# Performance work log

Measured on AMD Instinct MI355X. Metric: run time of the kernel, lower is better.

The kernel has to match this reference:

```python
import jax, jax.numpy as jnp
import numpy as np


def setup_inputs() -> dict:
    key = jax.random.key(0)
    x = jax.random.normal(key, (16, 2048, 512), dtype=jnp.float32)
    return {"x": x}


def reference(x):
    # Cosine (L2-normalized) self-attention.
    # norm: [B, N, 1] L2 norm over feature dim
    norm = jnp.sqrt(jnp.sum(x * x, axis=2, keepdims=True))
    # scores[b, i, j] = <x_i, x_j> / (|x_i| |x_j|)  -> [B, N, N]
    scores = jnp.einsum('bnd,bmd->bnm', x, x) / (norm * jnp.swapaxes(norm, -2, -1))
    p_attn = jax.nn.softmax(scores, axis=-1)
    # output: [B, N, D]
    return jnp.einsum('bnm,bmd->bnd', p_attn, x)
```

## Files before the change

kernel.cpp:

```cpp
#include <hip/hip_runtime.h>
#include <hip/hip_bf16.h>
#include <cstdint>
#include <cstddef>

#define BB 16
#define NN 2048
#define DD 512

typedef _Float16 f16x8 __attribute__((ext_vector_type(8)));
typedef _Float16 f16x4 __attribute__((ext_vector_type(4)));
typedef float f32x4 __attribute__((ext_vector_type(4)));

__device__ __forceinline__ void async_ld16(void* lds, const void* g) {
    __builtin_amdgcn_global_load_lds(
        (const __attribute__((address_space(1))) unsigned int*)(uintptr_t)g,
        (__attribute__((address_space(3))) unsigned int*)(uint32_t)(uintptr_t)lds,
        16, 0, 0);
}

#define VM_WAIT(n) asm volatile("s_waitcnt vmcnt(" #n ")" ::: "memory")
#define RAW_BAR()  do { asm volatile("" ::: "memory"); __builtin_amdgcn_s_barrier(); asm volatile("" ::: "memory"); } while (0)
#define LGKM_BAR() do { asm volatile("s_waitcnt lgkmcnt(0)" ::: "memory"); \
                        __builtin_amdgcn_s_barrier();                      \
                        __builtin_amdgcn_sched_barrier(0); } while (0)
#define LGKM0_FENCE() do { asm volatile("s_waitcnt lgkmcnt(0)" ::: "memory"); \
                           __builtin_amdgcn_sched_barrier(0); } while (0)

__global__ __launch_bounds__(256) void k_prep(const float* __restrict__ x,
                                              _Float16* __restrict__ xhn,
                                              _Float16* __restrict__ vT,
                                              float* __restrict__ denom) {
    __shared__ _Float16 t[512 * 66];
    const int tid = threadIdx.x, lane = tid & 63, w = tid >> 6;
    const int b = blockIdx.y, j0 = blockIdx.x * 64;
    if (tid < 64) denom[b * NN + j0 + tid] = 0.f;
    const float* xb = x + ((size_t)b * NN + j0) * DD;

    for (int rr = 0; rr < 16; ++rr) {
        const int jj = w * 16 + rr;
        const float* xr = xb + (size_t)jj * DD;
        float4 a = ((const float4*)xr)[lane];
        float4 c = ((const float4*)xr)[lane + 64];
        float ss = a.x*a.x + a.y*a.y + a.z*a.z + a.w*a.w
                 + c.x*c.x + c.y*c.y + c.z*c.z + c.w*c.w;
        #pragma unroll
        for (int o = 1; o < 64; o <<= 1) ss += __shfl_xor(ss, o);
        const float rn = 1.0f / sqrtf(ss);
        _Float16* dst = xhn + ((size_t)b * NN + j0 + jj) * DD;
        f16x4 v0 = {(_Float16)(a.x*rn), (_Float16)(a.y*rn), (_Float16)(a.z*rn), (_Float16)(a.w*rn)};
        f16x4 v1 = {(_Float16)(c.x*rn), (_Float16)(c.y*rn), (_Float16)(c.z*rn), (_Float16)(c.w*rn)};
        *(f16x4*)(dst + 4 * lane) = v0;
        *(f16x4*)(dst + 256 + 4 * lane) = v1;
        const int d0 = 4 * lane, d1 = 256 + 4 * lane;
        t[(d0 + 0) * 66 + jj] = (_Float16)a.x;
        t[(d0 + 1) * 66 + jj] = (_Float16)a.y;
        t[(d0 + 2) * 66 + jj] = (_Float16)a.z;
        t[(d0 + 3) * 66 + jj] = (_Float16)a.w;
        t[(d1 + 0) * 66 + jj] = (_Float16)c.x;
        t[(d1 + 1) * 66 + jj] = (_Float16)c.y;
        t[(d1 + 2) * 66 + jj] = (_Float16)c.z;
        t[(d1 + 3) * 66 + jj] = (_Float16)c.w;
    }
    LGKM_BAR();
    #pragma unroll
    for (int it = 0; it < 16; ++it) {
        const int id = it * 256 + tid;
        const int d = id >> 3, ch = (id & 7) * 8;
        const uint32_t* tp = (const uint32_t*)&t[d * 66 + ch];
        uint4 v = {tp[0], tp[1], tp[2], tp[3]};
        *(uint4*)(vT + ((size_t)b * DD + d) * NN + j0 + ch) = v;
    }
}

__global__ __launch_bounds__(256) void k_scores(const _Float16* __restrict__ xhn,
                                                _Float16* __restrict__ W,
                                                float* __restrict__ denom) {
    __shared__ _Float16 smem[32768];
    const int tid = threadIdx.x;
    const int lane = tid & 63, wv = tid >> 6;
    const int wr = wv >> 1, wc = wv & 1;
    const int m_ = lane & 15, quad = lane >> 4;
    const int b = blockIdx.z;

    const int swz = (blockIdx.x % 8) * 17 + blockIdx.x / 8;
    int rem = swz, ti = 0, rowlen = NN / 128;
    while (rem >= rowlen) { rem -= rowlen; ++ti; --rowlen; }
    const int tj = ti + rem;
    const int I = ti * 128, J = tj * 128;
    const bool diag = (ti == tj);

    const _Float16* Ab = xhn + ((size_t)b * NN + I) * DD;
    const _Float16* Bb = xhn + ((size_t)b * NN + J) * DD;

    f32x4 acc[4][4];
    #pragma unroll
    for (int i = 0; i < 4; ++i)
        #pragma unroll
        for (int j = 0; j < 4; ++j) acc[i][j] = (f32x4){0.f, 0.f, 0.f, 0.f};

    const int sub = lane >> 3;
    const int swc = (lane & 7) ^ sub;
    const _Float16* agl = Ab + (size_t)(wv * 32 + sub) * DD + swc * 8;
    const _Float16* bgl = Bb + (size_t)(wv * 32 + sub) * DD + swc * 8;

#define S_STAGE(kb_) do {                                                     \
    _Float16* A_ = smem + (((kb_) & 1) << 14);                                \
    const int k0_ = (kb_) * 64;                                               \
    _Pragma("unroll")                                                         \
    for (int c = 0; c < 4; ++c) {                                             \
        async_ld16(&A_[(wv * 32 + c * 8) * 64], agl + (size_t)c * 8 * DD + k0_); \
        async_ld16(&A_[8192 + (wv * 32 + c * 8) * 64], bgl + (size_t)c * 8 * DD + k0_); \
    } } while (0)

#define S_COMPUTE(kb_) do {                                                   \
    const _Float16* As_ = smem + (((kb_) & 1) << 14);                         \
    const _Float16* Bs_ = As_ + 8192;                                         \
    _Pragma("unroll")                                                         \
    for (int kc = 0; kc < 2; ++kc) {                                          \
        f16x8 af[4], bf[4];                                                   \
        _Pragma("unroll")                                                     \
        for (int t = 0; t < 4; ++t) {                                         \
            const int Ra = wr * 64 + t * 16 + m_;                             \
            const int Rb = wc * 64 + t * 16 + m_;                             \
            af[t] = *(const f16x8*)&As_[Ra * 64 + (((kc * 4 + quad) ^ (Ra & 7)) * 8)]; \
            bf[t] = *(const f16x8*)&Bs_[Rb * 64 + (((kc * 4 + quad) ^ (Rb & 7)) * 8)]; \
        }                                                                     \
        _Pragma("unroll")                                                     \
        for (int i = 0; i < 4; ++i)                                           \
            _Pragma("unroll")                                                 \
            for (int j = 0; j < 4; ++j)                                       \
                acc[i][j] = __builtin_amdgcn_mfma_f32_16x16x32_f16(af[i], bf[j], acc[i][j], 0, 0, 0); \
    } } while (0)

    S_STAGE(0); S_STAGE(1);
    for (int kb = 0; kb < DD / 64 - 1; ++kb) {
        VM_WAIT(8);
        RAW_BAR();
        __builtin_amdgcn_s_setprio(1);
        S_COMPUTE(kb);
        __builtin_amdgcn_s_setprio(0);
        RAW_BAR();
        if (kb + 2 < DD / 64) S_STAGE(kb + 2);
    }
    VM_WAIT(0);
    RAW_BAR();
    __builtin_amdgcn_s_setprio(1);
    S_COMPUTE(DD / 64 - 1);
    __builtin_amdgcn_s_setprio(0);

    f16x4 wq[4][4];
    float rowpart[4][4];
    float colpart[4] = {0.f, 0.f, 0.f, 0.f};
    #pragma unroll
    for (int i = 0; i < 4; ++i)
        #pragma unroll
        for (int r = 0; r < 4; ++r) rowpart[i][r] = 0.f;

    #pragma unroll
    for (int i = 0; i < 4; ++i) {
        #pragma unroll
        for (int j = 0; j < 4; ++j) {
            #pragma unroll
            for (int r = 0; r < 4; ++r) {
                const float w = __expf(acc[i][j][r]);
                wq[i][j][r] = (_Float16)w;
                rowpart[i][r] += w;
                colpart[j] += w;
            }
        }
    }

    #pragma unroll
    for (int i = 0; i < 4; ++i) {
        #pragma unroll
        for (int r = 0; r < 4; ++r) {
            float s = rowpart[i][r];
            s += __shfl_xor(s, 1);
            s += __shfl_xor(s, 2);
            s += __shfl_xor(s, 4);
            s += __shfl_xor(s, 8);
            if (m_ == 0)
                atomicAdd(&denom[b * NN + I + wr * 64 + i * 16 + quad * 4 + r], s);
        }
    }
    if (!diag) {
        #pragma unroll
        for (int j = 0; j < 4; ++j) {
            float s = colpart[j];
            s += __shfl_xor(s, 16);
            s += __shfl_xor(s, 32);
            if (quad == 0)
                atomicAdd(&denom[b * NN + J + wc * 64 + j * 16 + m_], s);
        }
    }

    LGKM_BAR();

    _Float16* WtT = smem;
    #pragma unroll
    for (int i = 0; i < 4; ++i) {
        const int rowb = wr * 64 + i * 16 + quad * 4;
        #pragma unroll
        for (int j = 0; j < 4; ++j) {
            const int col = wc * 64 + j * 16 + m_;
            *(f16x4*)&WtT[col * 136 + rowb] = wq[i][j];
        }
    }
    LGKM_BAR();
    #pragma unroll
    for (int it2 = 0; it2 < 8; ++it2) {
        const int id = it2 * 256 + tid;
        const int rr = id >> 4, off = (id & 15) * 8;
        *(uint4*)(W + ((size_t)b * NN + J + rr) * NN + I + off) =
            *(const uint4*)&WtT[rr * 136 + off];
    }
    if (!diag) {
        LGKM_BAR();
        _Float16* Wt = smem;
        #pragma unroll
        for (int i = 0; i < 4; ++i) {
            const int rowb = wr * 64 + i * 16 + quad * 4;
            #pragma unroll
            for (int j = 0; j < 4; ++j) {
                const int col = wc * 64 + j * 16 + m_;
                #pragma unroll
                for (int r = 0; r < 4; ++r)
                    Wt[(rowb + r) * 136 + col] = wq[i][j][r];
            }
        }
        LGKM_BAR();
        #pragma unroll
        for (int it2 = 0; it2 < 8; ++it2) {
            const int id = it2 * 256 + tid;
            const int rr = id >> 4, off = (id & 15) * 8;
            *(uint4*)(W + ((size_t)b * NN + I + rr) * NN + J + off) =
                *(const uint4*)&Wt[rr * 136 + off];
        }
    }
#undef S_STAGE
#undef S_COMPUTE
}

__global__ __launch_bounds__(512, 2) void k_pv(const _Float16* __restrict__ W,
                                               const _Float16* __restrict__ vT,
                                               const float* __restrict__ denom,
                                               float* __restrict__ out) {
    extern __shared__ _Float16 smem[];
    float* rdI = (float*)(smem + 65536);
    const int tid = threadIdx.x;
    const int lane = tid & 63, w = tid >> 6;
    const int wr = w >> 2, wcol = w & 3;
    const int m_ = lane & 15, quad = lane >> 4;

    const int bx = blockIdx.x;
    const int xcd = bx & 7, slot = bx >> 3;
    const int b  = (slot >> 4) * 8 + xcd;
    const int I  = ((slot >> 1) & 7) * 256;
    const int D0 = (slot & 1) * 256;

    const _Float16* Ab = W  + ((size_t)b * NN + I) * NN;
    const _Float16* Bb = vT + ((size_t)b * DD + D0) * NN;

    const int sub = lane >> 3;
    const int swc = (lane & 7) ^ sub;
    const _Float16* agl = Ab + (size_t)(w * 32 + sub) * NN + swc * 8;
    const _Float16* bgl = Bb + (size_t)(w * 32 + sub) * NN + swc * 8;

    f32x4 acc[8][4];
    #pragma unroll
    for (int i = 0; i < 8; ++i)
        #pragma unroll
        for (int j = 0; j < 4; ++j) acc[i][j] = (f32x4){0.f, 0.f, 0.f, 0.f};

    f16x8 afq[4][2];
    f16x8 bfq[4][2];

#define P_STAGE(kb_) do {                                                     \
    _Float16* A_ = smem + (((kb_) & 1) << 15);                                \
    const int k0_ = (kb_) * 64;                                               \
    _Pragma("unroll")                                                         \
    for (int c = 0; c < 4; ++c) {                                             \
        async_ld16(&A_[(w * 32 + c * 8) * 64], agl + (size_t)c * 8 * NN + k0_); \
        async_ld16(&A_[16384 + (w * 32 + c * 8) * 64], bgl + (size_t)c * 8 * NN + k0_); \
    } } while (0)

#define LD_A(t_, ih_) do {                                                    \
    const int R = wr * 128 + ((ih_) * 4 + (t_)) * 16 + m_;                    \
    afq[t_][0] = *(const f16x8*)&As_[R * 64 + ((quad ^ (R & 7)) * 8)];        \
    afq[t_][1] = *(const f16x8*)&As_[R * 64 + (((4 + quad) ^ (R & 7)) * 8)];  \
    } while (0)

#define LD_B(j_) do {                                                         \
    const int Rb = wcol * 64 + (j_) * 16 + m_;                                \
    bfq[j_][0] = *(const f16x8*)&Bs_[Rb * 64 + ((quad ^ (Rb & 7)) * 8)];      \
    bfq[j_][1] = *(const f16x8*)&Bs_[Rb * 64 + (((4 + quad) ^ (Rb & 7)) * 8)];\
    } while (0)

#define MFMA_Q(ih_, jh_) do {                                                 \
    __builtin_amdgcn_s_setprio(1);                                            \
    _Pragma("unroll")                                                         \
    for (int t = 0; t < 4; ++t)                                               \
        _Pragma("unroll")                                                     \
        for (int j = 0; j < 2; ++j) {                                         \
            acc[(ih_)*4+t][(jh_)*2+j] = __builtin_amdgcn_mfma_f32_16x16x32_f16( \
                afq[t][0], bfq[(jh_)*2+j][0], acc[(ih_)*4+t][(jh_)*2+j], 0, 0, 0); \
            acc[(ih_)*4+t][(jh_)*2+j] = __builtin_amdgcn_mfma_f32_16x16x32_f16( \
                afq[t][1], bfq[(jh_)*2+j][1], acc[(ih_)*4+t][(jh_)*2+j], 0, 0, 0); \
        }                                                                     \
    __builtin_amdgcn_s_setprio(0);                                            \
    } while (0)

    P_STAGE(0); P_STAGE(1);
    const int NT = NN / 64;
    for (int tc = 0; tc < NT; ++tc) {
        const _Float16* As_ = smem + ((tc & 1) << 15);
        const _Float16* Bs_ = As_ + 16384;
        if (tc == NT - 1) { VM_WAIT(0); } else { VM_WAIT(8); }
        RAW_BAR();
        #pragma unroll
        for (int t = 0; t < 4; ++t) LD_A(t, 0);
        LD_B(0); LD_B(1);
        RAW_BAR();
        LGKM0_FENCE();
        MFMA_Q(0, 0);
        RAW_BAR();
        LD_B(2); LD_B(3);
        RAW_BAR();
        LGKM0_FENCE();
        MFMA_Q(0, 1);
        RAW_BAR();
        #pragma unroll
        for (int t = 0; t < 4; ++t) LD_A(t, 1);
        RAW_BAR();
        LGKM0_FENCE();
        MFMA_Q(1, 0);
        RAW_BAR();
        if (tc + 2 < NT) P_STAGE(tc + 2);
        RAW_BAR();
        MFMA_Q(1, 1);
        RAW_BAR();
    }

    if (tid < 256) rdI[tid] = 1.0f / denom[b * NN + I + tid];
    LGKM_BAR();

    #pragma unroll
    for (int i = 0; i < 8; ++i) {
        const int rowb = wr * 128 + i * 16 + quad * 4;
        #pragma unroll
        for (int r = 0; r < 4; ++r) {
            const float sc = rdI[rowb + r];
            float* op = out + ((size_t)(b * NN + I + rowb + r)) * DD + D0;
            #pragma unroll
            for (int j = 0; j < 4; ++j)
                op[wcol * 64 + j * 16 + m_] = acc[i][j][r] * sc;
        }
    }
#undef P_STAGE
#undef LD_A
#undef LD_B
#undef MFMA_Q
}

extern "C" void kernel_launch(void* const* d_in, const int* in_sizes, int n_in,
                              void* d_out, int out_size, void* d_ws, size_t ws_size,
                              hipStream_t stream) {
    const float* x = (const float*)d_in[0];
    char* ws = (char*)d_ws;
    _Float16* xhn   = (_Float16*)(ws);
    _Float16* vT    = (_Float16*)(ws + (size_t)33554432);
    _Float16* W     = (_Float16*)(ws + (size_t)67108864);
    float*    denom = (float*)   (ws + (size_t)201326592);
    float*    out   = (float*)d_out;

    k_prep<<<dim3(NN / 64, BB), 256, 0, stream>>>(x, xhn, vT, denom);
    const int npairs = (NN / 128) * (NN / 128 + 1) / 2;
    k_scores<<<dim3(npairs, 1, BB), 256, 0, stream>>>(xhn, W, denom);
    k_pv<<<dim3(256, 1, 1), 512, 132096, stream>>>(W, vT, denom, out);
}
```

Baseline: 185.7 us.

## Single-buffer k_scores for occupancy and split k_pv prefetch across the loop

k_scores drops its double-buffered LDS pipeline for a single buffer, roughly halving shared memory. It adds launch_bounds(256,4) so more blocks can share a CU and hide load latency through occupancy instead of prefetch. k_pv splits each tile's async global-to-LDS staging into four parts spread across the MFMA phases, with the wait count adjusted, so load issue is interleaved with compute rather than bunched. The trade-off is that k_scores now stalls on every k-step and depends on the extra occupancy, which the register budget may not allow.

```diff
diff --git a/kernel.cpp b/kernel.cpp
--- a/kernel.cpp
+++ b/kernel.cpp
@@ -72,10 +72,10 @@
     }
 }
 
-__global__ __launch_bounds__(256) void k_scores(const _Float16* __restrict__ xhn,
-                                                _Float16* __restrict__ W,
-                                                float* __restrict__ denom) {
-    __shared__ _Float16 smem[32768];
+__global__ __launch_bounds__(256, 4) void k_scores(const _Float16* __restrict__ xhn,
+                                                   _Float16* __restrict__ W,
+                                                   float* __restrict__ denom) {
+    __shared__ _Float16 smem[17408];
     const int tid = threadIdx.x;
     const int lane = tid & 63, wv = tid >> 6;
     const int wr = wv >> 1, wc = wv & 1;
@@ -102,51 +102,38 @@
     const int swc = (lane & 7) ^ sub;
     const _Float16* agl = Ab + (size_t)(wv * 32 + sub) * DD + swc * 8;
     const _Float16* bgl = Bb + (size_t)(wv * 32 + sub) * DD + swc * 8;
-
-#define S_STAGE(kb_) do {                                                     \
-    _Float16* A_ = smem + (((kb_) & 1) << 14);                                \
-    const int k0_ = (kb_) * 64;                                               \
-    _Pragma("unroll")                                                         \
-    for (int c = 0; c < 4; ++c) {                                             \
-        async_ld16(&A_[(wv * 32 + c * 8) * 64], agl + (size_t)c * 8 * DD + k0_); \
-        async_ld16(&A_[8192 + (wv * 32 + c * 8) * 64], bgl + (size_t)c * 8 * DD + k0_); \
-    } } while (0)
-
-#define S_COMPUTE(kb_) do {                                                   \
-    const _Float16* As_ = smem + (((kb_) & 1) << 14);                         \
-    const _Float16* Bs_ = As_ + 8192;                                         \
-    _Pragma("unroll")                                                         \
-    for (int kc = 0; kc < 2; ++kc) {                                          \
-        f16x8 af[4], bf[4];                                                   \
-        _Pragma("unroll")                                                     \
-        for (int t = 0; t < 4; ++t) {                                         \
-            const int Ra = wr * 64 + t * 16 + m_;                             \
-            const int Rb = wc * 64 + t * 16 + m_;                             \
-            af[t] = *(const f16x8*)&As_[Ra * 64 + (((kc * 4 + quad) ^ (Ra & 7)) * 8)]; \
-            bf[t] = *(const f16x8*)&Bs_[Rb * 64 + (((kc * 4 + quad) ^ (Rb & 7)) * 8)]; \
-        }                                                                     \
-        _Pragma("unroll")                                                     \
-        for (int i = 0; i < 4; ++i)                                           \
-            _Pragma("unroll")                                                 \
-            for (int j = 0; j < 4; ++j)                                       \
-                acc[i][j] = __builtin_amdgcn_mfma_f32_16x16x32_f16(af[i], bf[j], acc[i][j], 0, 0, 0); \
-    } } while (0)
-
-    S_STAGE(0); S_STAGE(1);
-    for (int kb = 0; kb < DD / 64 - 1; ++kb) {
-        VM_WAIT(8);
+    _Float16* As = smem;
+    _Float16* Bs = smem + 8192;
+
+    for (int kb = 0; kb < DD / 64; ++kb) {
+        const int k0 = kb * 64;
+        #pragma unroll
+        for (int c = 0; c < 4; ++c) {
+            async_ld16(&As[(wv * 32 + c * 8) * 64], agl + (size_t)c * 8 * DD + k0);
+            async_ld16(&Bs[(wv * 32 + c * 8) * 64], bgl + (size_t)c * 8 * DD + k0);
+        }
+        VM_WAIT(0);
         RAW_BAR();
         __builtin_amdgcn_s_setprio(1);
-        S_COMPUTE(kb);
+        #pragma unroll
+        for (int kc = 0; kc < 2; ++kc) {
+            f16x8 af[4], bf[4];
+            #pragma unroll
+            for (int t = 0; t < 4; ++t) {
+                const int Ra = wr * 64 + t * 16 + m_;
+                const int Rb = wc * 64 + t * 16 + m_;
+                af[t] = *(const f16x8*)&As[Ra * 64 + (((kc * 4 + quad) ^ (Ra & 7)) * 8)];
+                bf[t] = *(const f16x8*)&Bs[Rb * 64 + (((kc * 4 + quad) ^ (Rb & 7)) * 8)];
+            }
+            #pragma unroll
+            for (int i = 0; i < 4; ++i)
+                #pragma unroll
+                for (int j = 0; j < 4; ++j)
+                    acc[i][j] = __builtin_amdgcn_mfma_f32_16x16x32_f16(af[i], bf[j], acc[i][j], 0, 0, 0);
+        }
         __builtin_amdgcn_s_setprio(0);
         RAW_BAR();
-        if (kb + 2 < DD / 64) S_STAGE(kb + 2);
-    }
-    VM_WAIT(0);
-    RAW_BAR();
-    __builtin_amdgcn_s_setprio(1);
-    S_COMPUTE(DD / 64 - 1);
-    __builtin_amdgcn_s_setprio(0);
+    }
 
     f16x4 wq[4][4];
     float rowpart[4][4];
@@ -237,8 +224,6 @@
                 *(const uint4*)&Wt[rr * 136 + off];
         }
     }
-#undef S_STAGE
-#undef S_COMPUTE
 }
 
 __global__ __launch_bounds__(512, 2) void k_pv(const _Float16* __restrict__ W,
@@ -275,14 +260,14 @@
     f16x8 afq[4][2];
     f16x8 bfq[4][2];
 
-#define P_STAGE(kb_) do {                                                     \
+    const int NT = NN / 64;
+
+#define P_PART(kb_, c_) do {                                                  \
     _Float16* A_ = smem + (((kb_) & 1) << 15);                                \
     const int k0_ = (kb_) * 64;                                               \
-    _Pragma("unroll")                                                         \
-    for (int c = 0; c < 4; ++c) {                                             \
-        async_ld16(&A_[(w * 32 + c * 8) * 64], agl + (size_t)c * 8 * NN + k0_); \
-        async_ld16(&A_[16384 + (w * 32 + c * 8) * 64], bgl + (size_t)c * 8 * NN + k0_); \
-    } } while (0)
+    async_ld16(&A_[(w * 32 + (c_) * 8) * 64], agl + (size_t)(c_) * 8 * NN + k0_); \
+    async_ld16(&A_[16384 + (w * 32 + (c_) * 8) * 64], bgl + (size_t)(c_) * 8 * NN + k0_); \
+    } while (0)
 
 #define LD_A(t_, ih_) do {                                                    \
     const int R = wr * 128 + ((ih_) * 4 + (t_)) * 16 + m_;                    \
@@ -310,21 +295,24 @@
     __builtin_amdgcn_s_setprio(0);                                            \
     } while (0)
 
-    P_STAGE(0); P_STAGE(1);
-    const int NT = NN / 64;
+    P_PART(0, 0); P_PART(0, 1); P_PART(0, 2); P_PART(0, 3);
+    P_PART(1, 0); P_PART(1, 1);
+
     for (int tc = 0; tc < NT; ++tc) {
         const _Float16* As_ = smem + ((tc & 1) << 15);
         const _Float16* Bs_ = As_ + 16384;
-        if (tc == NT - 1) { VM_WAIT(0); } else { VM_WAIT(8); }
+        if (tc == NT - 1) { VM_WAIT(0); } else { VM_WAIT(4); }
         RAW_BAR();
         #pragma unroll
         for (int t = 0; t < 4; ++t) LD_A(t, 0);
         LD_B(0); LD_B(1);
+        if (tc + 1 < NT) P_PART(tc + 1, 2);
         RAW_BAR();
         LGKM0_FENCE();
         MFMA_Q(0, 0);
         RAW_BAR();
         LD_B(2); LD_B(3);
+        if (tc + 1 < NT) P_PART(tc + 1, 3);
         RAW_BAR();
         LGKM0_FENCE();
         MFMA_Q(0, 1);
@@ -335,7 +323,7 @@
         LGKM0_FENCE();
         MFMA_Q(1, 0);
         RAW_BAR();
-        if (tc + 2 < NT) P_STAGE(tc + 2);
+        if (tc + 2 < NT) { P_PART(tc + 2, 0); P_PART(tc + 2, 1); }
         RAW_BAR();
         MFMA_Q(1, 1);
         RAW_BAR();
@@ -356,7 +344,7 @@
                 op[wcol * 64 + j * 16 + m_] = acc[i][j][r] * sc;
         }
     }
-#undef P_STAGE
+#undef P_PART
 #undef LD_A
 #undef LD_B
 #undef MFMA_Q
```

Measured after the change: 178.6 us. 1.04x faster.
